# Kernel tuning notes

Hardware: AMD Instinct MI355X
Metric: run time of the kernel (lower is better)

The kernel has to match this reference:

```python
import jax, jax.numpy as jnp
import numpy as np

N_NODES = 50000
N_EDGES = 400000
N_GRAPHS = 512
F = 32        # num_features
NB = 32       # mp_num_basis_fn
ZMAX = 118
CUTOFF = 5.0
NSPH = 9      # (mp_max_degree+1)^2 with max_degree=2
DEG_IDX = jnp.array([0, 1, 1, 1, 2, 2, 2, 2, 2])  # degree of each spherical component


def _bernstein(u, n=NB):
    # reciprocal_bernstein radial basis: Bernstein polynomials of degree n-1 at u in [0,1)
    k = jnp.arange(n, dtype=jnp.float32)
    log_binom = (jax.scipy.special.gammaln(float(n)) - jax.scipy.special.gammaln(k + 1.0)
                 - jax.scipy.special.gammaln(float(n) - k))
    u = jnp.clip(u, 1e-7, 1.0 - 1e-7)[..., None]
    return jnp.exp(log_binom + k * jnp.log(u) + (float(n) - 1.0 - k) * jnp.log1p(-u))


def _smooth_cutoff(r, cutoff=CUTOFF):
    t = r / cutoff
    return jnp.where(t < 1.0, jnp.exp(1.0 - 1.0 / jnp.clip(1.0 - t * t, 1e-7, None)), 0.0)


def _sph(u):
    # real spherical harmonics (cartesian normalization) up to degree 2; u: (E,3) unit vectors
    x, y, z = u[:, 0], u[:, 1], u[:, 2]
    c = jnp.sqrt(jnp.float32(3.0))
    return jnp.stack([jnp.ones_like(x), y, z, x,
                      c * x * y, c * y * z, 0.5 * (3.0 * z * z - 1.0),
                      c * z * x, 0.5 * c * (x * x - y * y)], axis=-1)


def _dense(x, W, b):
    # equivariant Dense: shared kernel over spherical components, bias only on scalar (l=0)
    y = jnp.einsum('nmf,fg->nmg', x, W)
    return y.at[:, 0, :].add(b)


def _silu_gate(x):
    # equivariant silu: scalar channel gates all degrees (scalar part -> exact silu)
    return x * jax.nn.sigmoid(x[:, 0:1, :])


def setup_inputs() -> dict:
    key = jax.random.key(0)
    ks = jax.random.split(key, 24)
    s = 1.0 / np.sqrt(F)
    sb = 1.0 / np.sqrt(NB)
    inp = {
        'positions': 2.0 * jax.random.normal(ks[0], (N_NODES, 3), jnp.float32),
        'embed': jax.random.normal(ks[1], (ZMAX, F), jnp.float32),
        'Wy0': sb * jax.random.normal(ks[2], (3, NB, F), jnp.float32),
        'Wx0': sb * jax.random.normal(ks[3], (3, NB, F), jnp.float32),
        'W1_0': s * jax.random.normal(ks[4], (F, F), jnp.float32),
        'b1_0': jnp.zeros((F,), jnp.float32),
        'W2_0': s * jax.random.normal(ks[5], (F, F), jnp.float32),
        'b2_0': jnp.zeros((F,), jnp.float32),
        'c0': jnp.full((1,), 0.5, jnp.float32),
        'Wr_last': sb * jax.random.normal(ks[6], (NB, F), jnp.float32),
        'W1_1': s * jax.random.normal(ks[7], (F, F), jnp.float32),
        'b1_1': jnp.zeros((F,), jnp.float32),
        'W2_1': s * jax.random.normal(ks[8], (F, F), jnp.float32),
        'b2_1': jnp.zeros((F,), jnp.float32),
        'c1': jnp.full((1,), 0.5, jnp.float32),
        'Wro1': s * jax.random.normal(ks[9], (F, F), jnp.float32),
        'bro1': jnp.zeros((F,), jnp.float32),
        'Wro2': s * jax.random.normal(ks[10], (F, 1), jnp.float32),
        'bro2': jnp.zeros((1,), jnp.float32),
        'atomic_bias': jax.random.normal(ks[11], (ZMAX,), jnp.float32),
        'atomic_numbers': jax.random.randint(ks[12], (N_NODES,), 0, ZMAX, jnp.int32),
        'dst_idx': jax.random.randint(ks[13], (N_EDGES,), 0, N_NODES, jnp.int32),
        'src_idx': jax.random.randint(ks[14], (N_EDGES,), 0, N_NODES, jnp.int32),
        'batch_segments': jnp.sort(jax.random.randint(ks[15], (N_NODES,), 0, N_GRAPHS, jnp.int32)),
        'graph_mask': jnp.ones((N_GRAPHS,), jnp.bool_),
    }
    return inp


def reference(positions, embed, Wy0, Wx0, W1_0, b1_0, W2_0, b2_0, c0,
              Wr_last, W1_1, b1_1, W2_1, b2_1, c1,
              Wro1, bro1, Wro2, bro2, atomic_bias,
              atomic_numbers, dst_idx, src_idx, batch_segments, graph_mask):
    # --- edge geometry (gather_src/gather_dst) ---
    disp = positions[src_idx] - positions[dst_idx]                # (E,3)
    r = jnp.sqrt(jnp.sum(disp * disp, axis=-1) + 1e-12)           # (E,)
    u = disp / r[:, None]
    Y = _sph(u)                                                   # (E,9)
    rbf = _bernstein(r / (r + 1.0)) * _smooth_cutoff(r)[:, None]  # (E,NB)

    # --- atomic embedding, lifted to (N, 9, F) with zero higher degrees ---
    x0 = embed[atomic_numbers]                                    # (N,F)
    x = jnp.concatenate([x0[:, None, :], jnp.zeros((N_NODES, NSPH - 1, F), x0.dtype)], axis=1)

    # --- iteration 0: full-degree equivariant message pass ---
    wy = jnp.einsum('eb,lbf->elf', rbf, Wy0)[:, DEG_IDX, :]       # (E,9,F) radial weights, (0,l)->l path
    wx = jnp.einsum('eb,lbf->elf', rbf, Wx0)[:, DEG_IDX, :]       # (l,0)->l path
    xs = x[src_idx]                                               # (E,9,F)
    msg = wy * Y[:, :, None] * xs[:, 0:1, :] + wx * xs
    y = jax.ops.segment_sum(msg, dst_idx, num_segments=N_NODES)   # (N,9,F)
    y = x + y
    y = _silu_gate(_dense(y, W1_0, b1_0))
    y = _dense(y, W2_0, b2_0)
    x = x + jax.nn.silu(c0) * y                                   # y_nl == 0 (era disabled)

    # --- iteration 1 (last): max_degree=0 message pass, then reduce to scalars ---
    w0 = rbf @ Wr_last                                            # (E,F)
    msg0 = w0 * x[src_idx, 0, :]
    y0 = jax.ops.segment_sum(msg0, dst_idx, num_segments=N_NODES) # (N,F)
    xs0 = x[:, 0, :]                                              # change_max_degree -> scalars
    y0 = xs0 + y0
    y0 = jax.nn.silu(y0 @ W1_1 + b1_1)
    y0 = y0 @ W2_1 + b2_1
    xs0 = xs0 + jax.nn.silu(c1) * y0

    # --- atomic readout and per-graph sum ---
    h = jax.nn.silu(xs0 @ Wro1 + bro1)
    e_atom = (h @ Wro2)[:, 0] + bro2[0] + atomic_bias[atomic_numbers]
    e_graph = jax.ops.segment_sum(e_atom, batch_segments, num_segments=N_GRAPHS)
    return jnp.where(graph_mask, e_graph, 0.0)
```

## Files before the change

kernel.cpp:

```cpp
#include <hip/hip_runtime.h>
#include <math.h>

#define NNODES 50000
#define NEDGES 400000
#define NGRAPHS 512
#define FDIM 32
#define CAP 64

static constexpr float BINOM31[32] = {
    1.f, 31.f, 465.f, 4495.f, 31465.f, 169911.f, 736281.f, 2629575.f,
    7888725.f, 20160075.f, 44352165.f, 84672315.f, 141120525.f, 206253075.f,
    265182525.f, 300540195.f, 300540195.f, 265182525.f, 206253075.f,
    141120525.f, 84672315.f, 44352165.f, 20160075.f, 7888725.f, 2629575.f,
    736281.f, 169911.f, 31465.f, 4495.f, 465.f, 31.f, 1.f
};

__device__ __forceinline__ float fast_rcp(float x) {
    return __builtin_amdgcn_rcpf(x);
}
__device__ __forceinline__ float silu(float x) {
    return x * fast_rcp(1.0f + __expf(-x));
}

__global__ __launch_bounds__(256) void build_csr(
    const float* __restrict__ pos,
    const int* __restrict__ srci, const int* __restrict__ dsti,
    const int* __restrict__ Z,
    float4* __restrict__ pay, int* __restrict__ deg,
    float* __restrict__ out)
{
    int e = blockIdx.x * 256 + threadIdx.x;
    if (e < NGRAPHS) out[e] = 0.0f;
    if (e >= NEDGES) return;
    int s = srci[e], d = dsti[e];
    float dx = pos[3 * s]     - pos[3 * d];
    float dy = pos[3 * s + 1] - pos[3 * d + 1];
    float dz = pos[3 * s + 2] - pos[3 * d + 2];
    float r = sqrtf(dx * dx + dy * dy + dz * dz + 1e-12f);
    if (r >= 5.0f) return;

    float t = r * 0.2f;
    float q = fmaxf(1.0f - t * t, 1e-7f);
    float cut = __expf(1.0f - fast_rcp(q));
    float v = fast_rcp(r + 1.0f);
    float v2 = v * v, v4 = v2 * v2, v8 = v4 * v4, v16 = v8 * v8;
    float scale = v16 * v8 * v4 * v2 * v * cut;

    int rank = atomicAdd(&deg[d], 1);
    if (rank < CAP)
        pay[(size_t)d * CAP + rank] =
            make_float4(r, scale, __int_as_float(s), __int_as_float(Z[s]));
}

#define DECLC(K) float C##K; { float _w = Wp1[K * FDIM + f];               \
                               if (Wp2) _w += Wp2[K * FDIM + f];           \
                               C##K = BINOM31[K] * _w; }
#define DECL_ALL_C                                                          \
    DECLC(0)  DECLC(1)  DECLC(2)  DECLC(3)  DECLC(4)  DECLC(5)  DECLC(6)   \
    DECLC(7)  DECLC(8)  DECLC(9)  DECLC(10) DECLC(11) DECLC(12) DECLC(13)  \
    DECLC(14) DECLC(15) DECLC(16) DECLC(17) DECLC(18) DECLC(19) DECLC(20)  \
    DECLC(21) DECLC(22) DECLC(23) DECLC(24) DECLC(25) DECLC(26) DECLC(27)  \
    DECLC(28) DECLC(29) DECLC(30) DECLC(31)

#define H8(K)                                                              \
    _w0 = fmaf(_w0, _p0.x, C##K); _w1 = fmaf(_w1, _p1.x, C##K);            \
    _w2 = fmaf(_w2, _p2.x, C##K); _w3 = fmaf(_w3, _p3.x, C##K);            \
    _w4 = fmaf(_w4, _p4.x, C##K); _w5 = fmaf(_w5, _p5.x, C##K);            \
    _w6 = fmaf(_w6, _p6.x, C##K); _w7 = fmaf(_w7, _p7.x, C##K);

#define GATHER_ACC8(XSRC, ROWSEL)                                          \
    float accv = 0.0f;                                                     \
    for (int j = 0; j < dg; j += 8) {                                      \
        int _j1 = min(j + 1, dg - 1), _j2 = min(j + 2, dg - 1);            \
        int _j3 = min(j + 3, dg - 1), _j4 = min(j + 4, dg - 1);            \
        int _j5 = min(j + 5, dg - 1), _j6 = min(j + 6, dg - 1);            \
        int _j7 = min(j + 7, dg - 1);                                      \
        float4 _p0 = slot[j];   float4 _p1 = slot[_j1];                    \
        float4 _p2 = slot[_j2]; float4 _p3 = slot[_j3];                    \
        float4 _p4 = slot[_j4]; float4 _p5 = slot[_j5];                    \
        float4 _p6 = slot[_j6]; float4 _p7 = slot[_j7];                    \
        float _s0 = _p0.y;                                                 \
        float _s1 = (j + 1 < dg) ? _p1.y : 0.f;                            \
        float _s2 = (j + 2 < dg) ? _p2.y : 0.f;                            \
        float _s3 = (j + 3 < dg) ? _p3.y : 0.f;                            \
        float _s4 = (j + 4 < dg) ? _p4.y : 0.f;                            \
        float _s5 = (j + 5 < dg) ? _p5.y : 0.f;                            \
        float _s6 = (j + 6 < dg) ? _p6.y : 0.f;                            \
        float _s7 = (j + 7 < dg) ? _p7.y : 0.f;                            \
        float _x0 = (XSRC)[(size_t)__float_as_int(_p0.ROWSEL) * FDIM + f]; \
        float _x1 = (XSRC)[(size_t)__float_as_int(_p1.ROWSEL) * FDIM + f]; \
        float _x2 = (XSRC)[(size_t)__float_as_int(_p2.ROWSEL) * FDIM + f]; \
        float _x3 = (XSRC)[(size_t)__float_as_int(_p3.ROWSEL) * FDIM + f]; \
        float _x4 = (XSRC)[(size_t)__float_as_int(_p4.ROWSEL) * FDIM + f]; \
        float _x5 = (XSRC)[(size_t)__float_as_int(_p5.ROWSEL) * FDIM + f]; \
        float _x6 = (XSRC)[(size_t)__float_as_int(_p6.ROWSEL) * FDIM + f]; \
        float _x7 = (XSRC)[(size_t)__float_as_int(_p7.ROWSEL) * FDIM + f]; \
        float _w0 = C31, _w1 = C31, _w2 = C31, _w3 = C31;                  \
        float _w4 = C31, _w5 = C31, _w6 = C31, _w7 = C31;                  \
        H8(30) H8(29) H8(28) H8(27) H8(26) H8(25) H8(24) H8(23)           \
        H8(22) H8(21) H8(20) H8(19) H8(18) H8(17) H8(16) H8(15)           \
        H8(14) H8(13) H8(12) H8(11) H8(10) H8(9)  H8(8)  H8(7)            \
        H8(6)  H8(5)  H8(4)  H8(3)  H8(2)  H8(1)  H8(0)                   \
        accv = fmaf(_s0 * _w0, _x0, accv);                                 \
        accv = fmaf(_s1 * _w1, _x1, accv);                                 \
        accv = fmaf(_s2 * _w2, _x2, accv);                                 \
        accv = fmaf(_s3 * _w3, _x3, accv);                                 \
        accv = fmaf(_s4 * _w4, _x4, accv);                                 \
        accv = fmaf(_s5 * _w5, _x5, accv);                                 \
        accv = fmaf(_s6 * _w6, _x6, accv);                                 \
        accv = fmaf(_s7 * _w7, _x7, accv);                                 \
    }

#define MATVEC32L(RES, WL, YP, BIAS) do {                                  \
    float4 _q0=(YP)[0], _q1=(YP)[1], _q2=(YP)[2], _q3=(YP)[3];             \
    float4 _q4=(YP)[4], _q5=(YP)[5], _q6=(YP)[6], _q7=(YP)[7];             \
    float _a0=(BIAS), _a1=0.f, _a2=0.f, _a3=0.f;                           \
    _a0=fmaf(_q0.x,(WL)[ 0*FDIM+f],_a0); _a0=fmaf(_q0.y,(WL)[ 1*FDIM+f],_a0); \
    _a0=fmaf(_q0.z,(WL)[ 2*FDIM+f],_a0); _a0=fmaf(_q0.w,(WL)[ 3*FDIM+f],_a0); \
    _a1=fmaf(_q1.x,(WL)[ 4*FDIM+f],_a1); _a1=fmaf(_q1.y,(WL)[ 5*FDIM+f],_a1); \
    _a1=fmaf(_q1.z,(WL)[ 6*FDIM+f],_a1); _a1=fmaf(_q1.w,(WL)[ 7*FDIM+f],_a1); \
    _a2=fmaf(_q2.x,(WL)[ 8*FDIM+f],_a2); _a2=fmaf(_q2.y,(WL)[ 9*FDIM+f],_a2); \
    _a2=fmaf(_q2.z,(WL)[10*FDIM+f],_a2); _a2=fmaf(_q2.w,(WL)[11*FDIM+f],_a2); \
    _a3=fmaf(_q3.x,(WL)[12*FDIM+f],_a3); _a3=fmaf(_q3.y,(WL)[13*FDIM+f],_a3); \
    _a3=fmaf(_q3.z,(WL)[14*FDIM+f],_a3); _a3=fmaf(_q3.w,(WL)[15*FDIM+f],_a3); \
    _a0=fmaf(_q4.x,(WL)[16*FDIM+f],_a0); _a0=fmaf(_q4.y,(WL)[17*FDIM+f],_a0); \
    _a0=fmaf(_q4.z,(WL)[18*FDIM+f],_a0); _a0=fmaf(_q4.w,(WL)[19*FDIM+f],_a0); \
    _a1=fmaf(_q5.x,(WL)[20*FDIM+f],_a1); _a1=fmaf(_q5.y,(WL)[21*FDIM+f],_a1); \
    _a1=fmaf(_q5.z,(WL)[22*FDIM+f],_a1); _a1=fmaf(_q5.w,(WL)[23*FDIM+f],_a1); \
    _a2=fmaf(_q6.x,(WL)[24*FDIM+f],_a2); _a2=fmaf(_q6.y,(WL)[25*FDIM+f],_a2); \
    _a2=fmaf(_q6.z,(WL)[26*FDIM+f],_a2); _a2=fmaf(_q6.w,(WL)[27*FDIM+f],_a2); \
    _a3=fmaf(_q7.x,(WL)[28*FDIM+f],_a3); _a3=fmaf(_q7.y,(WL)[29*FDIM+f],_a3); \
    _a3=fmaf(_q7.z,(WL)[30*FDIM+f],_a3); _a3=fmaf(_q7.w,(WL)[31*FDIM+f],_a3); \
    RES = (_a0+_a1)+(_a2+_a3); } while (0)

__global__ __launch_bounds__(256, 4) void fused_a(
    const float4* __restrict__ pay, const int* __restrict__ deg,
    const float* __restrict__ embed, const int* __restrict__ Z,
    const float* __restrict__ Wy0, const float* __restrict__ Wx0,
    const float* __restrict__ W1, const float* __restrict__ b1,
    const float* __restrict__ W2, const float* __restrict__ b2,
    const float* __restrict__ c0,
    float* __restrict__ x1buf)
{
    __shared__ __align__(16) float ylds[4][64];
    __shared__ float W1l[FDIM * FDIM];
    __shared__ float W2l[FDIM * FDIM];
    int tid = threadIdx.x;
    for (int i = tid; i < FDIM * FDIM; i += 256) {
        W1l[i] = W1[i];
        W2l[i] = W2[i];
    }
    __syncthreads();

    int widx = tid >> 6;
    int lane = tid & 63;
    int f    = lane & 31;
    int half = lane >> 5;

    const float* Wp1 = Wy0;
    const float* Wp2 = Wx0;
    DECL_ALL_C

    int n = (blockIdx.x * 4 + widx) * 2 + half;
    const float4* slot = pay + (size_t)n * CAP;
    int dg = min(deg[n], CAP);

    GATHER_ACC8(embed, w)

    float x0 = embed[Z[n] * FDIM + f];
    float yv = x0 + accv;

    float* yrow = &ylds[widx][half * 32];
    const float4* yp = (const float4*)yrow;
    yrow[f] = yv;
    float t;
    MATVEC32L(t, W1l, yp, b1[f]);
    t = silu(t);
    yrow[f] = t;
    float u;
    MATVEC32L(u, W2l, yp, b2[f]);
    x1buf[(size_t)n * FDIM + f] = fmaf(silu(c0[0]), u, x0);
}

__global__ __launch_bounds__(256, 4) void fused_b(
    const float4* __restrict__ pay, const int* __restrict__ deg,
    const float* __restrict__ x1buf, const float* __restrict__ Wr_last,
    const float* __restrict__ W1, const float* __restrict__ b1,
    const float* __restrict__ W2, const float* __restrict__ b2,
    const float* __restrict__ c1,
    const float* __restrict__ Wro1, const float* __restrict__ bro1,
    const float* __restrict__ Wro2, const float* __restrict__ bro2,
    const float* __restrict__ abias, const int* __restrict__ Z,
    const int* __restrict__ segs,
    float* __restrict__ out)
{
    __shared__ __align__(16) float ylds[4][64];
    __shared__ float W1l[FDIM * FDIM];
    __shared__ float W2l[FDIM * FDIM];
    __shared__ float Wrl[FDIM * FDIM];
    __shared__ float eb[8];
    __shared__ int   sb[8];
    int tid = threadIdx.x;
    for (int i = tid; i < FDIM * FDIM; i += 256) {
        W1l[i] = W1[i];
        W2l[i] = W2[i];
        Wrl[i] = Wro1[i];
    }
    __syncthreads();

    int widx = tid >> 6;
    int lane = tid & 63;
    int f    = lane & 31;
    int half = lane >> 5;

    const float* Wp1 = Wr_last;
    const float* Wp2 = nullptr;
    DECL_ALL_C

    int n = (blockIdx.x * 4 + widx) * 2 + half;
    const float4* slot = pay + (size_t)n * CAP;
    int dg = min(deg[n], CAP);

    GATHER_ACC8(x1buf, z)

    float x1 = x1buf[(size_t)n * FDIM + f];
    float yv = x1 + accv;

    float* yrow = &ylds[widx][half * 32];
    const float4* yp = (const float4*)yrow;
    yrow[f] = yv;
    float t;
    MATVEC32L(t, W1l, yp, b1[f]);
    t = silu(t);
    yrow[f] = t;
    float u;
    MATVEC32L(u, W2l, yp, b2[f]);
    float xs0 = fmaf(silu(c1[0]), u, x1);
    yrow[f] = xs0;
    float h;
    MATVEC32L(h, Wrl, yp, bro1[f]);
    float p = silu(h) * Wro2[f];
    p += __shfl_xor(p, 16, 32);
    p += __shfl_xor(p, 8, 32);
    p += __shfl_xor(p, 4, 32);
    p += __shfl_xor(p, 2, 32);
    p += __shfl_xor(p, 1, 32);

    if (f == 0) {
        eb[widx * 2 + half] = p + bro2[0] + abias[Z[n]];
        sb[widx * 2 + half] = segs[n];
    }
    __syncthreads();
    if (tid == 0) {
        float acc = eb[0];
        int cur = sb[0];
        #pragma unroll
        for (int i = 1; i < 8; ++i) {
            if (sb[i] == cur) acc += eb[i];
            else { atomicAdd(&out[cur], acc); cur = sb[i]; acc = eb[i]; }
        }
        atomicAdd(&out[cur], acc);
    }
}

extern "C" void kernel_launch(void* const* d_in, const int* in_sizes, int n_in,
                              void* d_out, int out_size, void* d_ws, size_t ws_size,
                              hipStream_t stream)
{
    const float* pos     = (const float*)d_in[0];
    const float* embed   = (const float*)d_in[1];
    const float* Wy0     = (const float*)d_in[2];
    const float* Wx0     = (const float*)d_in[3];
    const float* W1_0    = (const float*)d_in[4];
    const float* b1_0    = (const float*)d_in[5];
    const float* W2_0    = (const float*)d_in[6];
    const float* b2_0    = (const float*)d_in[7];
    const float* c0      = (const float*)d_in[8];
    const float* Wr_last = (const float*)d_in[9];
    const float* W1_1    = (const float*)d_in[10];
    const float* b1_1    = (const float*)d_in[11];
    const float* W2_1    = (const float*)d_in[12];
    const float* b2_1    = (const float*)d_in[13];
    const float* c1      = (const float*)d_in[14];
    const float* Wro1    = (const float*)d_in[15];
    const float* bro1    = (const float*)d_in[16];
    const float* Wro2    = (const float*)d_in[17];
    const float* bro2    = (const float*)d_in[18];
    const float* abias   = (const float*)d_in[19];
    const int*   Z       = (const int*)d_in[20];
    const int*   dsti    = (const int*)d_in[21];
    const int*   srci    = (const int*)d_in[22];
    const int*   segs    = (const int*)d_in[23];

    float* out = (float*)d_out;

    char* w = (char*)d_ws;
    float4* pay   = (float4*)w;  w += (size_t)NNODES * CAP * 16;
    float*  x1buf = (float*)w;   w += (size_t)NNODES * FDIM * 4;
    int*    deg   = (int*)w;     w += (size_t)NNODES * 4;

    hipMemsetAsync(deg, 0, NNODES * sizeof(int), stream);

    const int edgeBlocks = (NEDGES + 255) / 256;
    const int nodeBlocks = NNODES / 8;

    build_csr<<<edgeBlocks, 256, 0, stream>>>(pos, srci, dsti, Z, pay, deg, out);
    fused_a<<<nodeBlocks, 256, 0, stream>>>(pay, deg, embed, Z, Wy0, Wx0,
                                            W1_0, b1_0, W2_0, b2_0, c0, x1buf);
    fused_b<<<nodeBlocks, 256, 0, stream>>>(pay, deg, x1buf, Wr_last,
                                            W1_1, b1_1, W2_1, b2_1, c1,
                                            Wro1, bro1, Wro2, bro2,
                                            abias, Z, segs, out);
}
```

Before: 215.5 us.

## Split radial polynomial into even/odd Horner and pad positions to float4

The per-edge radial polynomial in the gather loop is now evaluated as two interleaved Horner chains in v² (even and odd coefficients), then combined with one fma. This halves the serial dependency depth, and the unroll drops from 8 to 4 edges per iteration, trading fewer in-flight gathers for lower register pressure. A new prep kernel replaces the memset: it zeroes the degree counters and output and copies positions into padded float4 so build_csr can fetch each endpoint with one vector load. This adds one kernel launch and a small extra buffer.

```diff
diff --git a/kernel.cpp b/kernel.cpp
--- a/kernel.cpp
+++ b/kernel.cpp
@@ -22,20 +22,30 @@
     return x * fast_rcp(1.0f + __expf(-x));
 }
 
+__global__ __launch_bounds__(256) void prep(
+    const float* __restrict__ pos, float4* __restrict__ pos4,
+    int* __restrict__ deg, float* __restrict__ out)
+{
+    int i = blockIdx.x * 256 + threadIdx.x;
+    if (i < NGRAPHS) out[i] = 0.0f;
+    if (i < NNODES) {
+        pos4[i] = make_float4(pos[3 * i], pos[3 * i + 1], pos[3 * i + 2], 0.f);
+        deg[i] = 0;
+    }
+}
+
 __global__ __launch_bounds__(256) void build_csr(
-    const float* __restrict__ pos,
+    const float4* __restrict__ pos4,
     const int* __restrict__ srci, const int* __restrict__ dsti,
     const int* __restrict__ Z,
-    float4* __restrict__ pay, int* __restrict__ deg,
-    float* __restrict__ out)
+    float4* __restrict__ pay, int* __restrict__ deg)
 {
     int e = blockIdx.x * 256 + threadIdx.x;
-    if (e < NGRAPHS) out[e] = 0.0f;
     if (e >= NEDGES) return;
     int s = srci[e], d = dsti[e];
-    float dx = pos[3 * s]     - pos[3 * d];
-    float dy = pos[3 * s + 1] - pos[3 * d + 1];
-    float dz = pos[3 * s + 2] - pos[3 * d + 2];
+    float4 ps = pos4[s];
+    float4 pd = pos4[d];
+    float dx = ps.x - pd.x, dy = ps.y - pd.y, dz = ps.z - pd.z;
     float r = sqrtf(dx * dx + dy * dy + dz * dz + 1e-12f);
     if (r >= 5.0f) return;
 
@@ -62,53 +72,43 @@
     DECLC(21) DECLC(22) DECLC(23) DECLC(24) DECLC(25) DECLC(26) DECLC(27)  \
     DECLC(28) DECLC(29) DECLC(30) DECLC(31)
 
-#define H8(K)                                                              \
-    _w0 = fmaf(_w0, _p0.x, C##K); _w1 = fmaf(_w1, _p1.x, C##K);            \
-    _w2 = fmaf(_w2, _p2.x, C##K); _w3 = fmaf(_w3, _p3.x, C##K);            \
-    _w4 = fmaf(_w4, _p4.x, C##K); _w5 = fmaf(_w5, _p5.x, C##K);            \
-    _w6 = fmaf(_w6, _p6.x, C##K); _w7 = fmaf(_w7, _p7.x, C##K);
-
-#define GATHER_ACC8(XSRC, ROWSEL)                                          \
+#define HEO(KE, KO)                                                        \
+    _ea = fmaf(_ea, _r2a, C##KE); _oa = fmaf(_oa, _r2a, C##KO);            \
+    _eb = fmaf(_eb, _r2b, C##KE); _ob = fmaf(_ob, _r2b, C##KO);            \
+    _ec = fmaf(_ec, _r2c, C##KE); _oc = fmaf(_oc, _r2c, C##KO);            \
+    _ed = fmaf(_ed, _r2d, C##KE); _od = fmaf(_od, _r2d, C##KO);
+
+#define GATHER_ACC4(XSRC, ROWSEL)                                          \
     float accv = 0.0f;                                                     \
-    for (int j = 0; j < dg; j += 8) {                                      \
-        int _j1 = min(j + 1, dg - 1), _j2 = min(j + 2, dg - 1);            \
-        int _j3 = min(j + 3, dg - 1), _j4 = min(j + 4, dg - 1);            \
-        int _j5 = min(j + 5, dg - 1), _j6 = min(j + 6, dg - 1);            \
-        int _j7 = min(j + 7, dg - 1);                                      \
-        float4 _p0 = slot[j];   float4 _p1 = slot[_j1];                    \
-        float4 _p2 = slot[_j2]; float4 _p3 = slot[_j3];                    \
-        float4 _p4 = slot[_j4]; float4 _p5 = slot[_j5];                    \
-        float4 _p6 = slot[_j6]; float4 _p7 = slot[_j7];                    \
-        float _s0 = _p0.y;                                                 \
-        float _s1 = (j + 1 < dg) ? _p1.y : 0.f;                            \
-        float _s2 = (j + 2 < dg) ? _p2.y : 0.f;                            \
-        float _s3 = (j + 3 < dg) ? _p3.y : 0.f;                            \
-        float _s4 = (j + 4 < dg) ? _p4.y : 0.f;                            \
-        float _s5 = (j + 5 < dg) ? _p5.y : 0.f;                            \
-        float _s6 = (j + 6 < dg) ? _p6.y : 0.f;                            \
-        float _s7 = (j + 7 < dg) ? _p7.y : 0.f;                            \
-        float _x0 = (XSRC)[(size_t)__float_as_int(_p0.ROWSEL) * FDIM + f]; \
-        float _x1 = (XSRC)[(size_t)__float_as_int(_p1.ROWSEL) * FDIM + f]; \
-        float _x2 = (XSRC)[(size_t)__float_as_int(_p2.ROWSEL) * FDIM + f]; \
-        float _x3 = (XSRC)[(size_t)__float_as_int(_p3.ROWSEL) * FDIM + f]; \
-        float _x4 = (XSRC)[(size_t)__float_as_int(_p4.ROWSEL) * FDIM + f]; \
-        float _x5 = (XSRC)[(size_t)__float_as_int(_p5.ROWSEL) * FDIM + f]; \
-        float _x6 = (XSRC)[(size_t)__float_as_int(_p6.ROWSEL) * FDIM + f]; \
-        float _x7 = (XSRC)[(size_t)__float_as_int(_p7.ROWSEL) * FDIM + f]; \
-        float _w0 = C31, _w1 = C31, _w2 = C31, _w3 = C31;                  \
-        float _w4 = C31, _w5 = C31, _w6 = C31, _w7 = C31;                  \
-        H8(30) H8(29) H8(28) H8(27) H8(26) H8(25) H8(24) H8(23)           \
-        H8(22) H8(21) H8(20) H8(19) H8(18) H8(17) H8(16) H8(15)           \
-        H8(14) H8(13) H8(12) H8(11) H8(10) H8(9)  H8(8)  H8(7)            \
-        H8(6)  H8(5)  H8(4)  H8(3)  H8(2)  H8(1)  H8(0)                   \
-        accv = fmaf(_s0 * _w0, _x0, accv);                                 \
-        accv = fmaf(_s1 * _w1, _x1, accv);                                 \
-        accv = fmaf(_s2 * _w2, _x2, accv);                                 \
-        accv = fmaf(_s3 * _w3, _x3, accv);                                 \
-        accv = fmaf(_s4 * _w4, _x4, accv);                                 \
-        accv = fmaf(_s5 * _w5, _x5, accv);                                 \
-        accv = fmaf(_s6 * _w6, _x6, accv);                                 \
-        accv = fmaf(_s7 * _w7, _x7, accv);                                 \
+    for (int j = 0; j < dg; j += 4) {                                      \
+        int _j1 = min(j + 1, dg - 1);                                      \
+        int _j2 = min(j + 2, dg - 1);                                      \
+        int _j3 = min(j + 3, dg - 1);                                      \
+        float4 _pa = slot[j];   float4 _pb = slot[_j1];                    \
+        float4 _pc = slot[_j2]; float4 _pd = slot[_j3];                    \
+        float _sa = _pa.y;                                                 \
+        float _sb = (j + 1 < dg) ? _pb.y : 0.f;                            \
+        float _sc = (j + 2 < dg) ? _pc.y : 0.f;                            \
+        float _sd = (j + 3 < dg) ? _pd.y : 0.f;                            \
+        float _xa = (XSRC)[(size_t)__float_as_int(_pa.ROWSEL) * FDIM + f]; \
+        float _xb = (XSRC)[(size_t)__float_as_int(_pb.ROWSEL) * FDIM + f]; \
+        float _xc = (XSRC)[(size_t)__float_as_int(_pc.ROWSEL) * FDIM + f]; \
+        float _xd = (XSRC)[(size_t)__float_as_int(_pd.ROWSEL) * FDIM + f]; \
+        float _r2a = _pa.x * _pa.x, _r2b = _pb.x * _pb.x;                  \
+        float _r2c = _pc.x * _pc.x, _r2d = _pd.x * _pd.x;                  \
+        float _ea = C30, _oa = C31, _eb = C30, _ob = C31;                  \
+        float _ec = C30, _oc = C31, _ed = C30, _od = C31;                  \
+        HEO(28, 29) HEO(26, 27) HEO(24, 25) HEO(22, 23) HEO(20, 21)       \
+        HEO(18, 19) HEO(16, 17) HEO(14, 15) HEO(12, 13) HEO(10, 11)       \
+        HEO(8, 9)   HEO(6, 7)   HEO(4, 5)   HEO(2, 3)   HEO(0, 1)         \
+        float _wa = fmaf(_pa.x, _oa, _ea);                                 \
+        float _wb = fmaf(_pb.x, _ob, _eb);                                 \
+        float _wc = fmaf(_pc.x, _oc, _ec);                                 \
+        float _wd = fmaf(_pd.x, _od, _ed);                                 \
+        accv = fmaf(_sa * _wa, _xa, accv);                                 \
+        accv = fmaf(_sb * _wb, _xb, accv);                                 \
+        accv = fmaf(_sc * _wc, _xc, accv);                                 \
+        accv = fmaf(_sd * _wd, _xd, accv);                                 \
     }
 
 #define MATVEC32L(RES, WL, YP, BIAS) do {                                  \
@@ -165,7 +165,7 @@
     const float4* slot = pay + (size_t)n * CAP;
     int dg = min(deg[n], CAP);
 
-    GATHER_ACC8(embed, w)
+    GATHER_ACC4(embed, w)
 
     float x0 = embed[Z[n] * FDIM + f];
     float yv = x0 + accv;
@@ -221,7 +221,7 @@
     const float4* slot = pay + (size_t)n * CAP;
     int dg = min(deg[n], CAP);
 
-    GATHER_ACC8(x1buf, z)
+    GATHER_ACC4(x1buf, z)
 
     float x1 = x1buf[(size_t)n * FDIM + f];
     float yv = x1 + accv;
@@ -297,14 +297,15 @@
     char* w = (char*)d_ws;
     float4* pay   = (float4*)w;  w += (size_t)NNODES * CAP * 16;
     float*  x1buf = (float*)w;   w += (size_t)NNODES * FDIM * 4;
+    float4* pos4  = (float4*)w;  w += (size_t)NNODES * 16;
     int*    deg   = (int*)w;     w += (size_t)NNODES * 4;
-
-    hipMemsetAsync(deg, 0, NNODES * sizeof(int), stream);
 
     const int edgeBlocks = (NEDGES + 255) / 256;
     const int nodeBlocks = NNODES / 8;
-
-    build_csr<<<edgeBlocks, 256, 0, stream>>>(pos, srci, dsti, Z, pay, deg, out);
+    const int prepBlocks = (NNODES + 255) / 256;
+
+    prep<<<prepBlocks, 256, 0, stream>>>(pos, pos4, deg, out);
+    build_csr<<<edgeBlocks, 256, 0, stream>>>(pos4, srci, dsti, Z, pay, deg);
     fused_a<<<nodeBlocks, 256, 0, stream>>>(pay, deg, embed, Z, Wy0, Wx0,
                                             W1_0, b1_0, W2_0, b2_0, c0, x1buf);
     fused_b<<<nodeBlocks, 256, 0, stream>>>(pay, deg, x1buf, Wr_last,
```

Result: faster. 204.7 us (-5.0%).
